# Kernel tuning notes

Measured on AMD Instinct MI355X. Metric: run time of the kernel, lower is better.

Reference implementation:

```python
import jax, jax.numpy as jnp
import numpy as np

N = 100000
E = 1600000
F_IN = 128
H1, C1 = 8, 8          # conv1: 8 heads x 8 channels -> 64
H2, C2 = 1, 16         # conv2: 1 head x num_classes
NEG_SLOPE = 0.2


def setup_inputs() -> dict:
    key = jax.random.key(0)
    ks = jax.random.split(key, 10)
    x = jax.random.normal(ks[0], (N, F_IN), dtype=jnp.float32)
    edge_index = jax.random.randint(ks[1], (2, E), 0, N, dtype=jnp.int64)
    s = 0.1
    return {
        "x": x,
        "edge_index": edge_index,
        "W1": jax.random.normal(ks[2], (F_IN, H1 * C1), dtype=jnp.float32) * s,
        "att_src1": jax.random.normal(ks[3], (H1, C1), dtype=jnp.float32) * s,
        "att_dst1": jax.random.normal(ks[4], (H1, C1), dtype=jnp.float32) * s,
        "b1": jnp.zeros((H1 * C1,), dtype=jnp.float32),
        "W2": jax.random.normal(ks[5], (H1 * C1, H2 * C2), dtype=jnp.float32) * s,
        "att_src2": jax.random.normal(ks[6], (H2, C2), dtype=jnp.float32) * s,
        "att_dst2": jax.random.normal(ks[7], (H2, C2), dtype=jnp.float32) * s,
        "b2": jnp.zeros((H2 * C2,), dtype=jnp.float32),
    }


def gat_conv(x, src, dst, W, a_src, a_dst, bias, heads, out_ch):
    n = x.shape[0]
    h = (x @ W).reshape(n, heads, out_ch)            # [N,H,C]
    alpha_s = jnp.einsum("nhc,hc->nh", h, a_src)      # [N,H]
    alpha_d = jnp.einsum("nhc,hc->nh", h, a_dst)
    e = jax.nn.leaky_relu(alpha_s[src] + alpha_d[dst], NEG_SLOPE)  # [Etot,H]
    # segment softmax over edges grouped by destination node
    e_max = jax.ops.segment_max(e, dst, num_segments=n)
    w = jnp.exp(e - e_max[dst])
    denom = jax.ops.segment_sum(w, dst, num_segments=n)
    alpha = w / denom[dst]                            # [Etot,H]
    msg = h[src] * alpha[:, :, None]                  # [Etot,H,C]
    out = jax.ops.segment_sum(msg, dst, num_segments=n)
    return out.reshape(n, heads * out_ch) + bias


def reference(x, edge_index, W1, att_src1, att_dst1, b1, W2, att_src2, att_dst2, b2):
    # PyG GATConv adds self-loops by default
    loops = jnp.arange(N, dtype=edge_index.dtype)
    src = jnp.concatenate([edge_index[0], loops])
    dst = jnp.concatenate([edge_index[1], loops])
    # dropout layers are identity in eval mode
    h = gat_conv(x, src, dst, W1, att_src1, att_dst1, b1, H1, C1)
    h = jax.nn.elu(h)
    out = gat_conv(h, src, dst, W2, att_src2, att_dst2, b2, H2, C2)
    return out
```

## Files before the change

### kernel.cpp

```cpp
#include <hip/hip_runtime.h>

#define NEG_SLOPE 0.2f
#define BKT 64
#define SHIFT 9
#define CAP 10240

typedef __attribute__((ext_vector_type(8))) short bf16x8;
typedef __attribute__((ext_vector_type(4))) float f32x4;

__device__ __forceinline__ unsigned short f2bf(float f) {
    unsigned u = __float_as_uint(f);
    return (unsigned short)((u + 0x7FFFu + ((u >> 16) & 1u)) >> 16);
}
__device__ __forceinline__ float bf2f(unsigned short h) {
    return __uint_as_float((unsigned)h << 16);
}
__device__ __forceinline__ unsigned pack_bf16(float a, float b) {
    unsigned ua = __float_as_uint(a), ub = __float_as_uint(b);
    ua = (ua + 0x7FFFu + ((ua >> 16) & 1u)) >> 16;
    ub = (ub + 0x7FFFu + ((ub >> 16) & 1u)) & 0xFFFF0000u;
    return ua | ub;
}
__device__ __forceinline__ float bflo(unsigned v) { return __uint_as_float(v << 16); }
__device__ __forceinline__ float bfhi(unsigned v) { return __uint_as_float(v & 0xFFFF0000u); }

__global__ void wext_kernel(const float* __restrict__ W1, const float* __restrict__ as_,
                            const float* __restrict__ ad_, unsigned short* __restrict__ wext) {
    int i = blockIdx.x * 256 + threadIdx.x;
    if (i >= 128 * 80) return;
    int k = i / 80, c = i % 80;
    float v;
    if (c < 64) {
        v = W1[k * 64 + c];
    } else if (c < 72) {
        int h = c - 64; v = 0.f;
        for (int q = 0; q < 8; ++q) v += W1[k * 64 + h * 8 + q] * as_[h * 8 + q];
    } else {
        int h = c - 72; v = 0.f;
        for (int q = 0; q < 8; ++q) v += W1[k * 64 + h * 8 + q] * ad_[h * 8 + q];
    }
    wext[i] = f2bf(v);
}

__global__ __launch_bounds__(256) void fat_kernel(
    const float* __restrict__ x, const unsigned short* __restrict__ wext,
    unsigned* __restrict__ h1bf, float* __restrict__ as1, float* __restrict__ ad1,
    const int* __restrict__ src, const int* __restrict__ dst,
    int* __restrict__ cursor, int* __restrict__ bucket,
    int* __restrict__ gcur, int2* __restrict__ binned,
    int n, int ntiles, int gemm_blocks, int E, int Etot, int nbins, int mode) {
    if ((int)blockIdx.x < gemm_blocks) {
        int lane = threadIdx.x & 63;
        int r = lane & 15, g = lane >> 4;
        bf16x8 wf[4][5];
#pragma unroll
        for (int ks = 0; ks < 4; ++ks)
#pragma unroll
            for (int nt = 0; nt < 5; ++nt) {
                const unsigned short* wp = wext + (size_t)(ks * 32 + g * 8) * 80 + nt * 16 + r;
#pragma unroll
                for (int i = 0; i < 8; ++i) wf[ks][nt][i] = (short)wp[(size_t)i * 80];
            }
        int nwaves = gemm_blocks * 4;
        int w = blockIdx.x * 4 + (threadIdx.x >> 6);
        for (int t = w; t < ntiles; t += nwaves) {
            int row = t * 16 + r;
            int rowc = row < n ? row : n - 1;
            const float* xp = x + (size_t)rowc * 128 + g * 8;
            float4 fa[4], fb[4];
#pragma unroll
            for (int ks = 0; ks < 4; ++ks) {
                fa[ks] = *(const float4*)(xp + ks * 32);
                fb[ks] = *(const float4*)(xp + ks * 32 + 4);
            }
            f32x4 acc[5];
#pragma unroll
            for (int nt = 0; nt < 5; ++nt) acc[nt] = (f32x4){0.f, 0.f, 0.f, 0.f};
#pragma unroll
            for (int ks = 0; ks < 4; ++ks) {
                float f[8];
                f[0] = fa[ks].x; f[1] = fa[ks].y; f[2] = fa[ks].z; f[3] = fa[ks].w;
                f[4] = fb[ks].x; f[5] = fb[ks].y; f[6] = fb[ks].z; f[7] = fb[ks].w;
                bf16x8 ah, al;
#pragma unroll
                for (int i = 0; i < 8; ++i) {
                    unsigned short hb = f2bf(f[i]);
                    ah[i] = (short)hb;
                    al[i] = (short)f2bf(f[i] - bf2f(hb));
                }
#pragma unroll
                for (int nt = 0; nt < 5; ++nt)
                    acc[nt] = __builtin_amdgcn_mfma_f32_16x16x32_bf16(ah, wf[ks][nt], acc[nt], 0, 0, 0);
#pragma unroll
                for (int nt = 0; nt < 5; ++nt)
                    acc[nt] = __builtin_amdgcn_mfma_f32_16x16x32_bf16(al, wf[ks][nt], acc[nt], 0, 0, 0);
            }
#pragma unroll
            for (int reg = 0; reg < 4; ++reg) {
                int nrow = t * 16 + g * 4 + reg;
                bool live = nrow < n;
#pragma unroll
                for (int nt = 0; nt < 4; ++nt) {
                    float v = acc[nt][reg];
                    float o = __shfl_xor(v, 1, 64);
                    if (live && !(r & 1))
                        h1bf[(size_t)nrow * 32 + nt * 8 + (r >> 1)] = pack_bf16(v, o);
                }
                float v4 = acc[4][reg];
                if (live) {
                    if (r < 8) as1[(size_t)nrow * 8 + r] = v4;
                    else       ad1[(size_t)nrow * 8 + (r - 8)] = v4;
                }
            }
        }
    } else if (mode == 2) {
        __shared__ int lhist[256];
        __shared__ int lbase[256];
        int t = threadIdx.x;
        int blk = (int)blockIdx.x - gemm_blocks;
        lhist[t] = 0;
        __syncthreads();
        int e0 = blk * 2048;
        int d[8], s[8], lo[8];
        bool val[8];
#pragma unroll
        for (int j = 0; j < 8; ++j) {
            int e = e0 + j * 256 + t;
            val[j] = e < Etot;
            d[j] = s[j] = 0;
            if (val[j]) {
                if (e < E) { s[j] = src[e]; d[j] = dst[e]; }
                else { s[j] = d[j] = e - E; }
                lo[j] = atomicAdd(&lhist[d[j] >> SHIFT], 1);
            }
        }
        __syncthreads();
        if (t < nbins && lhist[t] > 0) lbase[t] = atomicAdd(&gcur[t], lhist[t]);
        __syncthreads();
#pragma unroll
        for (int j = 0; j < 8; ++j) {
            if (val[j]) {
                int bin = d[j] >> SHIFT;
                int pos = lbase[bin] + lo[j];
                if (pos < CAP) binned[(size_t)bin * CAP + pos] = make_int2(d[j], s[j]);
            }
        }
    } else {
        int tid = ((int)blockIdx.x - gemm_blocks) * 256 + threadIdx.x;
        int T = ((int)gridDim.x - gemm_blocks) * 256;
        int s[8], d[8], p[8];
        bool v[8];
#pragma unroll
        for (int j = 0; j < 8; ++j) {
            int e = tid + j * T;
            v[j] = e < Etot;
            s[j] = d[j] = 0;
            if (v[j]) {
                if (e < E) { s[j] = src[e]; d[j] = dst[e]; }
                else { s[j] = d[j] = e - E; }
            }
        }
#pragma unroll
        for (int j = 0; j < 8; ++j)
            if (v[j]) p[j] = atomicAdd(&cursor[d[j]], 1);
#pragma unroll
        for (int j = 0; j < 8; ++j)
            if (v[j] && p[j] < BKT) bucket[(size_t)d[j] * BKT + p[j]] = s[j];
    }
}

__global__ __launch_bounds__(512) void binB_kernel(const int* __restrict__ gcur,
                                                   const int2* __restrict__ binned,
                                                   int* __restrict__ bucket,
                                                   int* __restrict__ cursor, int n) {
    __shared__ int lcur[512];
    int bin = blockIdx.x;
    int t = threadIdx.x;
    lcur[t] = 0;
    __syncthreads();
    int cnt = gcur[bin];
    if (cnt > CAP) cnt = CAP;
    const int2* bp = binned + (size_t)bin * CAP;
    for (int k = t; k < cnt; k += 512) {
        int2 p = bp[k];
        int slot = atomicAdd(&lcur[p.x & 511], 1);
        if (slot < BKT) bucket[(size_t)p.x * BKT + slot] = p.y;
    }
    __syncthreads();
    int node = (bin << SHIFT) + t;
    if (node < n) cursor[node] = min(lcur[t], BKT);
}

__global__ void agg1_kernel(const int* __restrict__ cursor, const int* __restrict__ edges,
                            const float* __restrict__ as1, const float* __restrict__ ad1,
                            const uint4* __restrict__ h1bf4, const float* __restrict__ b1,
                            const float* __restrict__ W2, const float* __restrict__ as2w,
                            const float* __restrict__ ad2w, unsigned* __restrict__ h2bf,
                            float* __restrict__ as2, float* __restrict__ ad2, int n) {
    __shared__ float sW[64 * 17];
    __shared__ int eds[8][64];
    for (int i = threadIdx.x; i < 64 * 16; i += blockDim.x)
        sW[(i >> 4) * 17 + (i & 15)] = W2[i];
    __syncthreads();
    int wave = (blockIdx.x * blockDim.x + threadIdx.x) >> 6;
    int pair = wave * 2;
    if (pair >= n) return;
    int lane = threadIdx.x & 63;
    int wv = threadIdx.x >> 6;
    int half = lane >> 5;
    int slot = wv * 2 + half;
    int hbase = lane & 32;
    int l5 = lane & 31, g = l5 >> 3, u = l5 & 7;
    int node = pair + half;
    bool valid = node < n;
    int nodec = valid ? node : pair;
    int cnt = valid ? min(cursor[nodec], BKT) : 0;
    const int* ed = edges + (size_t)nodec * BKT;
    eds[slot][l5] = ed[l5];
    eds[slot][32 + l5] = ed[32 + l5];
    float adv = ad1[(size_t)nodec * 8 + u];
    int cntmax = max(cnt, __shfl_xor(cnt, 32, 64));
    float a0 = 0.f, a1 = 0.f, a2 = 0.f, a3 = 0.f;
    float a4 = 0.f, a5 = 0.f, a6 = 0.f, a7 = 0.f, wsum = 0.f;
    for (int k0 = 0; k0 < cntmax; k0 += 8) {
        int k1 = k0 + g, k2 = k0 + 4 + g;
        int s1 = eds[slot][k1 & 63];
        int s2 = eds[slot][k2 & 63];
        if (k1 < cnt) {
            float a = as1[(size_t)s1 * 8 + u] + adv;
            float ee = a > 0.f ? a : NEG_SLOPE * a;
            float w = __expf(ee);
            uint4 v = h1bf4[(size_t)s1 * 8 + u];
            a0 += w * bflo(v.x); a1 += w * bfhi(v.x);
            a2 += w * bflo(v.y); a3 += w * bfhi(v.y);
            a4 += w * bflo(v.z); a5 += w * bfhi(v.z);
            a6 += w * bflo(v.w); a7 += w * bfhi(v.w);
            wsum += w;
        }
        if (k2 < cnt) {
            float a = as1[(size_t)s2 * 8 + u] + adv;
            float ee = a > 0.f ? a : NEG_SLOPE * a;
            float w = __expf(ee);
            uint4 v = h1bf4[(size_t)s2 * 8 + u];
            a0 += w * bflo(v.x); a1 += w * bfhi(v.x);
            a2 += w * bflo(v.y); a3 += w * bfhi(v.y);
            a4 += w * bflo(v.z); a5 += w * bfhi(v.z);
            a6 += w * bflo(v.w); a7 += w * bfhi(v.w);
            wsum += w;
        }
    }
#pragma unroll
    for (int off = 8; off <= 16; off <<= 1) {
        a0 += __shfl_xor(a0, off, 64); a1 += __shfl_xor(a1, off, 64);
        a2 += __shfl_xor(a2, off, 64); a3 += __shfl_xor(a3, off, 64);
        a4 += __shfl_xor(a4, off, 64); a5 += __shfl_xor(a5, off, 64);
        a6 += __shfl_xor(a6, off, 64); a7 += __shfl_xor(a7, off, 64);
        wsum += __shfl_xor(wsum, off, 64);
    }
    float inv = 1.f / wsum;
    float4 bb0 = ((const float4*)b1)[2 * u];
    float4 bb1 = ((const float4*)b1)[2 * u + 1];
    float e0 = a0 * inv + bb0.x, e1 = a1 * inv + bb0.y;
    float e2 = a2 * inv + bb0.z, e3 = a3 * inv + bb0.w;
    float e4 = a4 * inv + bb1.x, e5 = a5 * inv + bb1.y;
    float e6 = a6 * inv + bb1.z, e7 = a7 * inv + bb1.w;
    e0 = e0 > 0.f ? e0 : __expf(e0) - 1.f;
    e1 = e1 > 0.f ? e1 : __expf(e1) - 1.f;
    e2 = e2 > 0.f ? e2 : __expf(e2) - 1.f;
    e3 = e3 > 0.f ? e3 : __expf(e3) - 1.f;
    e4 = e4 > 0.f ? e4 : __expf(e4) - 1.f;
    e5 = e5 > 0.f ? e5 : __expf(e5) - 1.f;
    e6 = e6 > 0.f ? e6 : __expf(e6) - 1.f;
    e7 = e7 > 0.f ? e7 : __expf(e7) - 1.f;
    int gg = l5 >> 4, c = l5 & 15;
    float hv = 0.f;
#pragma unroll
    for (int m = 0; m < 4; ++m) {
        int usrc = hbase + 4 * gg + m;
        int rbase = (4 * gg + m) * 8;
        float q;
        q = __shfl(e0, usrc, 64); hv += q * sW[(rbase + 0) * 17 + c];
        q = __shfl(e1, usrc, 64); hv += q * sW[(rbase + 1) * 17 + c];
        q = __shfl(e2, usrc, 64); hv += q * sW[(rbase + 2) * 17 + c];
        q = __shfl(e3, usrc, 64); hv += q * sW[(rbase + 3) * 17 + c];
        q = __shfl(e4, usrc, 64); hv += q * sW[(rbase + 4) * 17 + c];
        q = __shfl(e5, usrc, 64); hv += q * sW[(rbase + 5) * 17 + c];
        q = __shfl(e6, usrc, 64); hv += q * sW[(rbase + 6) * 17 + c];
        q = __shfl(e7, usrc, 64); hv += q * sW[(rbase + 7) * 17 + c];
    }
    hv += __shfl_xor(hv, 16, 64);
    float v0 = __shfl(hv, hbase + 2 * u, 64);
    float v1 = __shfl(hv, hbase + 2 * u + 1, 64);
    if (valid && l5 < 8) h2bf[(size_t)node * 8 + l5] = pack_bf16(v0, v1);
    float ts = hv * as2w[c], td = hv * ad2w[c];
    ts += __shfl_xor(ts, 1, 64); td += __shfl_xor(td, 1, 64);
    ts += __shfl_xor(ts, 2, 64); td += __shfl_xor(td, 2, 64);
    ts += __shfl_xor(ts, 4, 64); td += __shfl_xor(td, 4, 64);
    ts += __shfl_xor(ts, 8, 64); td += __shfl_xor(td, 8, 64);
    if (valid && l5 == 0) { as2[node] = ts; ad2[node] = td; }
}

__global__ void agg2_kernel(const int* __restrict__ cursor, const int* __restrict__ edges,
                            const float* __restrict__ as2, const float* __restrict__ ad2,
                            const uint2* __restrict__ h2bf2, const float* __restrict__ b2,
                            float* __restrict__ out, int n) {
    int gtid = blockIdx.x * blockDim.x + threadIdx.x;
    int node = gtid >> 6;
    int lane = threadIdx.x & 63;
    if (node >= n) return;
    int g = lane >> 2, u = lane & 3;
    int cnt = min(cursor[node], BKT);
    const int* ed = edges + (size_t)node * BKT;
    int ed_reg = ed[lane];
    float adv = ad2[node];
    float a0 = 0.f, a1 = 0.f, a2 = 0.f, a3 = 0.f, wsum = 0.f;
#pragma unroll
    for (int i = 0; i < 4; ++i) {
        int k = i * 16 + g;
        int s = __shfl(ed_reg, k, 64);
        if (k < cnt) {
            float a = as2[s] + adv;
            float ee = a > 0.f ? a : NEG_SLOPE * a;
            float w = __expf(ee);
            uint2 v = h2bf2[(size_t)s * 4 + u];
            a0 += w * bflo(v.x);
            a1 += w * bfhi(v.x);
            a2 += w * bflo(v.y);
            a3 += w * bfhi(v.y);
            wsum += w;
        }
    }
#pragma unroll
    for (int off = 4; off <= 32; off <<= 1) {
        a0 += __shfl_xor(a0, off, 64); a1 += __shfl_xor(a1, off, 64);
        a2 += __shfl_xor(a2, off, 64); a3 += __shfl_xor(a3, off, 64);
        wsum += __shfl_xor(wsum, off, 64);
    }
    if (lane < 4) {
        float inv = 1.f / wsum;
        float4 bb = ((const float4*)b2)[u];
        ((float4*)out)[(size_t)node * 4 + u] =
            make_float4(a0 * inv + bb.x, a1 * inv + bb.y, a2 * inv + bb.z, a3 * inv + bb.w);
    }
}

extern "C" void kernel_launch(void* const* d_in, const int* in_sizes, int n_in,
                              void* d_out, int out_size, void* d_ws, size_t ws_size,
                              hipStream_t stream) {
    const float* x      = (const float*)d_in[0];
    const int*   ei     = (const int*)d_in[1];
    const float* W1     = (const float*)d_in[2];
    const float* att_s1 = (const float*)d_in[3];
    const float* att_d1 = (const float*)d_in[4];
    const float* b1     = (const float*)d_in[5];
    const float* W2     = (const float*)d_in[6];
    const float* att_s2 = (const float*)d_in[7];
    const float* att_d2 = (const float*)d_in[8];
    const float* b2     = (const float*)d_in[9];

    int N_   = in_sizes[0] / 128;
    int E_   = in_sizes[1] / 2;
    int Etot = E_ + N_;
    const int* srcA = ei;
    const int* dstA = ei + E_;

    unsigned short* wext = (unsigned short*)d_ws;
    unsigned* h1bf = (unsigned*)(wext + 128 * 80);
    float* as1   = (float*)(h1bf + (size_t)N_ * 32);
    float* ad1   = as1 + (size_t)N_ * 8;
    unsigned* h2bf = (unsigned*)(ad1 + (size_t)N_ * 8);
    float* as2   = (float*)(h2bf + (size_t)N_ * 8);
    float* ad2   = as2 + (size_t)N_;
    int*   cursor = (int*)(ad2 + (size_t)N_);
    int*   bucket = cursor + N_;
    int*   gcur   = bucket + (size_t)N_ * BKT;
    int2*  binned = (int2*)(gcur + 256);

    int nbins = (N_ + (1 << SHIFT) - 1) >> SHIFT;
    size_t need_bucket = 20480 + (size_t)N_ * (32 + 8 + 8 + 8 + 1 + 1 + 1 + BKT) * 4;
    size_t need_binned = need_bucket + 1024 + (size_t)nbins * CAP * 8;
    bool use_bucket = ws_size >= need_bucket;
    bool use_binned = (ws_size >= need_binned) && (nbins <= 256);

    int ntiles = (N_ + 15) / 16;
    int GB1 = (ntiles + 15) / 16;
    int GB2 = (Etot + 2047) / 2048;
    int nb_wave  = ((size_t)N_ * 64 + 255) / 256;
    int nb_pair  = (N_ + 7) / 8;

    wext_kernel<<<40, 256, 0, stream>>>(W1, att_s1, att_d1, wext);

    if (use_binned) {
        hipMemsetAsync(gcur, 0, (size_t)nbins * sizeof(int), stream);
        fat_kernel<<<GB1 + GB2, 256, 0, stream>>>(x, wext, h1bf, as1, ad1, srcA, dstA,
                                                  cursor, bucket, gcur, binned,
                                                  N_, ntiles, GB1, E_, Etot, nbins, 2);
        binB_kernel<<<nbins, 512, 0, stream>>>(gcur, binned, bucket, cursor, N_);
    } else if (use_bucket) {
        hipMemsetAsync(cursor, 0, (size_t)N_ * sizeof(int), stream);
        fat_kernel<<<GB1 + GB2, 256, 0, stream>>>(x, wext, h1bf, as1, ad1, srcA, dstA,
                                                  cursor, bucket, nullptr, nullptr,
                                                  N_, ntiles, GB1, E_, Etot, nbins, 1);
    } else {
        return;
    }

    agg1_kernel<<<nb_pair, 256, 0, stream>>>(cursor, bucket, as1, ad1,
                                             (const uint4*)h1bf, b1, W2, att_s2, att_d2,
                                             h2bf, as2, ad2, N_);
    agg2_kernel<<<nb_wave, 256, 0, stream>>>(cursor, bucket, as2, ad2,
                                             (const uint2*)h2bf, b2, (float*)d_out, N_);
}
```

Measured before the change: 152.9 us.

## Pack binned edges to 32-bit and build compact CSR rows per bin

The binning pass now stores each edge as one packed 32-bit word (source shifted left, local destination in the low bits) instead of an int2 pair, which halves binned traffic. binB counts edges per node, runs a shared-memory prefix scan, and writes a compact CSR-like edge array plus per-node (offset, count) rowinfo, replacing the fixed 64-slot padded bucket. The aggregation kernels read rowinfo and load only the valid edge entries, cutting reads of padded bucket memory. The cost is an extra counting pass and a log-step scan with many barriers in binB, and an added guard that N fits in the packing width.

```diff
diff --git a/kernel.cpp b/kernel.cpp
--- a/kernel.cpp
+++ b/kernel.cpp
@@ -47,7 +47,7 @@
     unsigned* __restrict__ h1bf, float* __restrict__ as1, float* __restrict__ ad1,
     const int* __restrict__ src, const int* __restrict__ dst,
     int* __restrict__ cursor, int* __restrict__ bucket,
-    int* __restrict__ gcur, int2* __restrict__ binned,
+    int* __restrict__ gcur, unsigned* __restrict__ binnedP,
     int n, int ntiles, int gemm_blocks, int E, int Etot, int nbins, int mode) {
     if ((int)blockIdx.x < gemm_blocks) {
         int lane = threadIdx.x & 63;
@@ -142,7 +142,9 @@
             if (val[j]) {
                 int bin = d[j] >> SHIFT;
                 int pos = lbase[bin] + lo[j];
-                if (pos < CAP) binned[(size_t)bin * CAP + pos] = make_int2(d[j], s[j]);
+                if (pos < CAP)
+                    binnedP[(size_t)bin * CAP + pos] =
+                        ((unsigned)s[j] << SHIFT) | (unsigned)(d[j] & ((1 << SHIFT) - 1));
             }
         }
     } else {
@@ -170,28 +172,46 @@
 }
 
 __global__ __launch_bounds__(512) void binB_kernel(const int* __restrict__ gcur,
-                                                   const int2* __restrict__ binned,
-                                                   int* __restrict__ bucket,
-                                                   int* __restrict__ cursor, int n) {
-    __shared__ int lcur[512];
+                                                   const unsigned* __restrict__ binnedP,
+                                                   int* __restrict__ bucketC,
+                                                   int2* __restrict__ rowinfo, int n) {
+    __shared__ int lcnt[512];
+    __shared__ int loff[512];
     int bin = blockIdx.x;
     int t = threadIdx.x;
-    lcur[t] = 0;
+    lcnt[t] = 0;
     __syncthreads();
     int cnt = gcur[bin];
     if (cnt > CAP) cnt = CAP;
-    const int2* bp = binned + (size_t)bin * CAP;
+    const unsigned* bp = binnedP + (size_t)bin * CAP;
+    for (int k = t; k < cnt; k += 512)
+        atomicAdd(&lcnt[bp[k] & 511], 1);
+    __syncthreads();
+    int myc = lcnt[t];
+    for (int off = 1; off < 512; off <<= 1) {
+        int tv = (t >= off) ? lcnt[t - off] : 0;
+        __syncthreads();
+        lcnt[t] += tv;
+        __syncthreads();
+    }
+    int excl = lcnt[t] - myc;
+    loff[t] = excl;
+    __syncthreads();
+    lcnt[t] = 0;
+    int base = bin * CAP;
+    int node = (bin << SHIFT) + t;
+    if (node < n) rowinfo[node] = make_int2(base + excl, min(myc, BKT));
+    __syncthreads();
     for (int k = t; k < cnt; k += 512) {
-        int2 p = bp[k];
-        int slot = atomicAdd(&lcur[p.x & 511], 1);
-        if (slot < BKT) bucket[(size_t)p.x * BKT + slot] = p.y;
-    }
-    __syncthreads();
-    int node = (bin << SHIFT) + t;
-    if (node < n) cursor[node] = min(lcur[t], BKT);
-}
-
-__global__ void agg1_kernel(const int* __restrict__ cursor, const int* __restrict__ edges,
+        unsigned v = bp[k];
+        int loc = v & 511;
+        int slot = atomicAdd(&lcnt[loc], 1);
+        if (slot < BKT) bucketC[base + loff[loc] + slot] = (int)(v >> SHIFT);
+    }
+}
+
+__global__ void agg1_kernel(const int2* __restrict__ rowinfo, const int* __restrict__ cursor,
+                            const int* __restrict__ edges,
                             const float* __restrict__ as1, const float* __restrict__ ad1,
                             const uint4* __restrict__ h1bf4, const float* __restrict__ b1,
                             const float* __restrict__ W2, const float* __restrict__ as2w,
@@ -214,10 +234,18 @@
     int node = pair + half;
     bool valid = node < n;
     int nodec = valid ? node : pair;
-    int cnt = valid ? min(cursor[nodec], BKT) : 0;
-    const int* ed = edges + (size_t)nodec * BKT;
-    eds[slot][l5] = ed[l5];
-    eds[slot][32 + l5] = ed[32 + l5];
+    int row, cnt;
+    if (rowinfo) {
+        int2 rc = rowinfo[nodec];
+        row = rc.x;
+        cnt = valid ? rc.y : 0;
+    } else {
+        row = nodec * BKT;
+        cnt = valid ? min(cursor[nodec], BKT) : 0;
+    }
+    const int* ed = edges + row;
+    eds[slot][l5] = (l5 < cnt) ? ed[l5] : 0;
+    if (l5 + 32 < cnt) eds[slot][32 + l5] = ed[32 + l5];
     float adv = ad1[(size_t)nodec * 8 + u];
     int cntmax = max(cnt, __shfl_xor(cnt, 32, 64));
     float a0 = 0.f, a1 = 0.f, a2 = 0.f, a3 = 0.f;
@@ -300,7 +328,8 @@
     if (valid && l5 == 0) { as2[node] = ts; ad2[node] = td; }
 }
 
-__global__ void agg2_kernel(const int* __restrict__ cursor, const int* __restrict__ edges,
+__global__ void agg2_kernel(const int2* __restrict__ rowinfo, const int* __restrict__ cursor,
+                            const int* __restrict__ edges,
                             const float* __restrict__ as2, const float* __restrict__ ad2,
                             const uint2* __restrict__ h2bf2, const float* __restrict__ b2,
                             float* __restrict__ out, int n) {
@@ -309,9 +338,16 @@
     int lane = threadIdx.x & 63;
     if (node >= n) return;
     int g = lane >> 2, u = lane & 3;
-    int cnt = min(cursor[node], BKT);
-    const int* ed = edges + (size_t)node * BKT;
-    int ed_reg = ed[lane];
+    int row, cnt;
+    if (rowinfo) {
+        int2 rc = rowinfo[node];
+        row = rc.x; cnt = rc.y;
+    } else {
+        row = node * BKT;
+        cnt = min(cursor[node], BKT);
+    }
+    const int* ed = edges + row;
+    int ed_reg = (lane < cnt) ? ed[lane] : 0;
     float adv = ad2[node];
     float a0 = 0.f, a1 = 0.f, a2 = 0.f, a3 = 0.f, wsum = 0.f;
 #pragma unroll
@@ -372,15 +408,17 @@
     float* as2   = (float*)(h2bf + (size_t)N_ * 8);
     float* ad2   = as2 + (size_t)N_;
     int*   cursor = (int*)(ad2 + (size_t)N_);
-    int*   bucket = cursor + N_;
+    int2*  rowinfo = (int2*)(cursor + N_);
+    int*   bucket = (int*)(rowinfo + N_);
     int*   gcur   = bucket + (size_t)N_ * BKT;
-    int2*  binned = (int2*)(gcur + 256);
+    unsigned* binnedP = (unsigned*)(gcur + 256);
+    int*   bucketC = (int*)(binnedP + (size_t)256 * CAP);
 
     int nbins = (N_ + (1 << SHIFT) - 1) >> SHIFT;
-    size_t need_bucket = 20480 + (size_t)N_ * (32 + 8 + 8 + 8 + 1 + 1 + 1 + BKT) * 4;
-    size_t need_binned = need_bucket + 1024 + (size_t)nbins * CAP * 8;
+    size_t need_bucket = 20480 + (size_t)N_ * (32 + 8 + 8 + 8 + 1 + 1 + 1 + 2 + BKT) * 4;
+    size_t need_binned = need_bucket + 1024 + (size_t)256 * CAP * 8;
     bool use_bucket = ws_size >= need_bucket;
-    bool use_binned = (ws_size >= need_binned) && (nbins <= 256);
+    bool use_binned = (ws_size >= need_binned) && (nbins <= 256) && (N_ <= (1 << 22));
 
     int ntiles = (N_ + 15) / 16;
     int GB1 = (ntiles + 15) / 16;
@@ -393,21 +431,23 @@
     if (use_binned) {
         hipMemsetAsync(gcur, 0, (size_t)nbins * sizeof(int), stream);
         fat_kernel<<<GB1 + GB2, 256, 0, stream>>>(x, wext, h1bf, as1, ad1, srcA, dstA,
-                                                  cursor, bucket, gcur, binned,
+                                                  cursor, bucket, gcur, binnedP,
                                                   N_, ntiles, GB1, E_, Etot, nbins, 2);
-        binB_kernel<<<nbins, 512, 0, stream>>>(gcur, binned, bucket, cursor, N_);
+        binB_kernel<<<nbins, 512, 0, stream>>>(gcur, binnedP, bucketC, rowinfo, N_);
+        agg1_kernel<<<nb_pair, 256, 0, stream>>>(rowinfo, cursor, bucketC, as1, ad1,
+                                                 (const uint4*)h1bf, b1, W2, att_s2, att_d2,
+                                                 h2bf, as2, ad2, N_);
+        agg2_kernel<<<nb_wave, 256, 0, stream>>>(rowinfo, cursor, bucketC, as2, ad2,
+                                                 (const uint2*)h2bf, b2, (float*)d_out, N_);
     } else if (use_bucket) {
         hipMemsetAsync(cursor, 0, (size_t)N_ * sizeof(int), stream);
         fat_kernel<<<GB1 + GB2, 256, 0, stream>>>(x, wext, h1bf, as1, ad1, srcA, dstA,
                                                   cursor, bucket, nullptr, nullptr,
                                                   N_, ntiles, GB1, E_, Etot, nbins, 1);
-    } else {
-        return;
-    }
-
-    agg1_kernel<<<nb_pair, 256, 0, stream>>>(cursor, bucket, as1, ad1,
-                                             (const uint4*)h1bf, b1, W2, att_s2, att_d2,
-                                             h2bf, as2, ad2, N_);
-    agg2_kernel<<<nb_wave, 256, 0, stream>>>(cursor, bucket, as2, ad2,
-                                             (const uint2*)h2bf, b2, (float*)d_out, N_);
-}
+        agg1_kernel<<<nb_pair, 256, 0, stream>>>(nullptr, cursor, bucket, as1, ad1,
+                                                 (const uint4*)h1bf, b1, W2, att_s2, att_d2,
+                                                 h2bf, as2, ad2, N_);
+        agg2_kernel<<<nb_wave, 256, 0, stream>>>(nullptr, cursor, bucket, as2, ad2,
+                                                 (const uint2*)h2bf, b2, (float*)d_out, N_);
+    }
+}
```

After: 157.9 us. 3.3% more time.
